# Performance work log

Hardware: AMD Instinct MI355X
Metric: run time of the kernel (lower is better)

## Reference

```python
import jax, jax.numpy as jnp
import numpy as np

EMBED_DIM = 512
NUM_HEADS = 8
HEAD_DIM = EMBED_DIM // NUM_HEADS  # 64
LN_EPS = 1e-5
SEQ = 2048
BATCH = 2


def sparsemax(z):
    """Sparsemax over last axis: euclidean projection of each row onto the simplex."""
    K = z.shape[-1]
    z_sorted = -jnp.sort(-z, axis=-1)                      # descending
    z_cumsum = jnp.cumsum(z_sorted, axis=-1)
    r = jnp.arange(1, K + 1, dtype=z.dtype)
    support = r * z_sorted > (z_cumsum - 1.0)
    k_int = jnp.sum(support.astype(jnp.int32), axis=-1, keepdims=True)  # support size >= 1
    tau_sum = jnp.take_along_axis(z_cumsum, k_int - 1, axis=-1)
    tau = (tau_sum - 1.0) / k_int.astype(z.dtype)
    return jnp.maximum(z - tau, 0.0)


def layer_norm(x, eps=LN_EPS):
    # per-head pattern normalization over head_dim, no affine (normalize_pattern_affine=False)
    mu = jnp.mean(x, axis=-1, keepdims=True)
    var = jnp.mean(jnp.square(x - mu), axis=-1, keepdims=True)
    return (x - mu) * jax.lax.rsqrt(var + eps)


def setup_inputs() -> dict:
    key = jax.random.key(0)
    ks = jax.random.split(key, 6)
    E = EMBED_DIM
    return {
        "query": jax.random.normal(ks[0], (SEQ, BATCH, E), dtype=jnp.float32),
        "key": jax.random.normal(ks[1], (SEQ, BATCH, E), dtype=jnp.float32),
        "value": jax.random.normal(ks[2], (SEQ, BATCH, E), dtype=jnp.float32),
        "in_proj_weight": 0.02 * jax.random.normal(ks[3], (3 * E, E), dtype=jnp.float32),
        "in_proj_bias": jnp.zeros((3 * E,), dtype=jnp.float32),
        "out_proj_weight": 0.02 * jax.random.normal(ks[4], (E, E), dtype=jnp.float32),
        "out_proj_bias": jnp.zeros((E,), dtype=jnp.float32),
        "update_steps_max": 0,  # single association pass
    }


def reference(query, key, value, in_proj_weight, in_proj_bias,
              out_proj_weight, out_proj_bias, update_steps_max):
    L, B, E = query.shape
    S = key.shape[0]
    H, D = NUM_HEADS, HEAD_DIM
    wq, wk, wv = in_proj_weight[:E], in_proj_weight[E:2 * E], in_proj_weight[2 * E:]
    bq, bk, bv = in_proj_bias[:E], in_proj_bias[E:2 * E], in_proj_bias[2 * E:]
    # projections (torch Linear: x @ W.T + b)
    q = (query @ wq.T + bq).reshape(L, B, H, D)
    k = (key @ wk.T + bk).reshape(S, B, H, D)
    v = (value @ wv.T + bv).reshape(S, B, H, D)
    # pattern normalization (normalize_pattern=True, no affine), then attention scaling
    q = layer_norm(q) * (float(D) ** -0.5)
    k = layer_norm(k)
    v = layer_norm(v)
    # association scores [B, H, Lq, Lk]
    scores = jnp.einsum('ibhd,jbhd->bhij', q, k)
    attn = sparsemax(scores)  # sparse='sparsemax' activation over key axis
    out = jnp.einsum('bhij,jbhd->ibhd', attn, v).reshape(L, B, E)
    return out @ out_proj_weight.T + out_proj_bias
```

## Files before the change

### kernel.cpp

```cpp
#include <hip/hip_runtime.h>

#define SEQ   2048
#define BATCH 2
#define EMB   512
#define NH    8
#define HD    64
#define CAP   48

typedef short bf16x8 __attribute__((ext_vector_type(8)));
typedef float f32x4  __attribute__((ext_vector_type(4)));

static __device__ __forceinline__ unsigned short f2bf(float f) {
    unsigned u = __float_as_uint(f);
    unsigned r = (u + 0x7FFF + ((u >> 16) & 1)) >> 16;
    return (unsigned short)r;
}
static __device__ __forceinline__ float bf2f(unsigned short h) {
    return __uint_as_float((unsigned)h << 16);
}

__global__ __launch_bounds__(256) void gemm_qkv_ln(
    const float* __restrict__ query, const float* __restrict__ key_in,
    const float* __restrict__ value,
    const float* __restrict__ ipw, const float* __restrict__ ipb,
    unsigned short* __restrict__ qhi, unsigned short* __restrict__ qlo,
    unsigned short* __restrict__ khi, unsigned short* __restrict__ klo,
    float* __restrict__ vn)
{
    const int z = blockIdx.z;
    const float* X = (z == 0) ? query : (z == 1) ? key_in : value;
    unsigned short* dh = (z == 0) ? qhi : khi;
    unsigned short* dl = (z == 0) ? qlo : klo;
    const float scale = (z == 0) ? 0.125f : 1.0f;

    const int t0  = blockIdx.x * 128;
    const int h   = blockIdx.y;
    const int og0 = z * EMB + h * 64;

    __shared__ float Xs[16][132];
    __shared__ float Ws[16][68];
    __shared__ float Et[128][68];
    __shared__ float mu_s[128], rs_s[128];

    const int tid = threadIdx.x;
    const int tx  = tid & 15;
    const int ty  = tid >> 4;

    float acc[8][4];
#pragma unroll
    for (int i = 0; i < 8; ++i)
#pragma unroll
        for (int j = 0; j < 4; ++j) acc[i][j] = 0.f;

    for (int ck = 0; ck < 32; ++ck) {
        const int c0 = ck * 16;
#pragma unroll
        for (int p = 0; p < 2; ++p) {
            int f  = tid + p * 256;
            int tl = f >> 2, cq = (f & 3) << 2;
            const float4 v = *(const float4*)&X[(size_t)(t0 + tl) * EMB + c0 + cq];
            Xs[cq + 0][tl] = v.x; Xs[cq + 1][tl] = v.y;
            Xs[cq + 2][tl] = v.z; Xs[cq + 3][tl] = v.w;
        }
        {
            int f  = tid;
            int ol = f >> 2, cq = (f & 3) << 2;
            const float4 v = *(const float4*)&ipw[(size_t)(og0 + ol) * EMB + c0 + cq];
            Ws[cq + 0][ol] = v.x; Ws[cq + 1][ol] = v.y;
            Ws[cq + 2][ol] = v.z; Ws[cq + 3][ol] = v.w;
        }
        __syncthreads();
#pragma unroll
        for (int c = 0; c < 16; ++c) {
            const float4 a0 = *(const float4*)&Xs[c][ty * 8];
            const float4 a1 = *(const float4*)&Xs[c][ty * 8 + 4];
            const float4 b  = *(const float4*)&Ws[c][tx * 4];
            const float av[8] = {a0.x, a0.y, a0.z, a0.w, a1.x, a1.y, a1.z, a1.w};
            const float bv[4] = {b.x, b.y, b.z, b.w};
#pragma unroll
            for (int i = 0; i < 8; ++i)
#pragma unroll
                for (int j = 0; j < 4; ++j) acc[i][j] += av[i] * bv[j];
        }
        __syncthreads();
    }

#pragma unroll
    for (int j = 0; j < 4; ++j) {
        const float bj = ipb[og0 + tx * 4 + j];
#pragma unroll
        for (int i = 0; i < 8; ++i) Et[ty * 8 + i][tx * 4 + j] = acc[i][j] + bj;
    }
    __syncthreads();
    if (tid < 128) {
        float s = 0.f;
#pragma unroll
        for (int dq = 0; dq < 64; dq += 4) {
            const float4 v = *(const float4*)&Et[tid][dq];
            s += v.x + v.y + v.z + v.w;
        }
        const float mu = s * (1.0f / 64.0f);
        float vs = 0.f;
#pragma unroll
        for (int dq = 0; dq < 64; dq += 4) {
            const float4 v = *(const float4*)&Et[tid][dq];
            const float a = v.x - mu, b = v.y - mu, c = v.z - mu, d = v.w - mu;
            vs += a * a + b * b + c * c + d * d;
        }
        mu_s[tid] = mu;
        rs_s[tid] = rsqrtf(vs * (1.0f / 64.0f) + 1e-5f);
    }
    __syncthreads();
#pragma unroll
    for (int p = 0; p < 8; ++p) {
        int f  = tid + p * 256;
        int tl = f >> 4, dq = (f & 15) << 2;
        const float4 v = *(const float4*)&Et[tl][dq];
        const float mu = mu_s[tl];
        const float rs = rs_s[tl] * scale;
        float x0 = (v.x - mu) * rs, x1 = (v.y - mu) * rs;
        float x2 = (v.z - mu) * rs, x3 = (v.w - mu) * rs;
        const int tg = t0 + tl;
        const int ii = tg >> 1;
        const int b  = tg & 1;
        const size_t base = ((size_t)(b * NH + h) * SEQ + ii) * 64 + dq;
        if (z == 2) {
            float4 o; o.x = x0; o.y = x1; o.z = x2; o.w = x3;
            *(float4*)&vn[base] = o;
        } else {
            ushort4 hi, lo;
            hi.x = f2bf(x0); lo.x = f2bf(x0 - bf2f(hi.x));
            hi.y = f2bf(x1); lo.y = f2bf(x1 - bf2f(hi.y));
            hi.z = f2bf(x2); lo.z = f2bf(x2 - bf2f(hi.z));
            hi.w = f2bf(x3); lo.w = f2bf(x3 - bf2f(hi.w));
            *(ushort4*)&dh[base] = hi;
            *(ushort4*)&dl[base] = lo;
        }
    }
}

__global__ __launch_bounds__(512, 4) void attn_sparsemax_mfma(
    const unsigned short* __restrict__ qhi, const unsigned short* __restrict__ qlo,
    const unsigned short* __restrict__ khi, const unsigned short* __restrict__ klo,
    const float* __restrict__ vn, float* __restrict__ ao)
{
    __shared__ float          plist[16][8][CAP];
    __shared__ unsigned short jlist[16][8][CAP];
    __shared__ short          lcnt[16][8];
    __shared__ float          wred[8][16];
    __shared__ float          wcnt[8][16];
    __shared__ float          O_lds[16][64];

    const int tid = threadIdx.x;
    const int w   = tid >> 6;
    const int l   = tid & 63;
    const int c   = l & 15;
    const int g   = l >> 4;
    const int bh  = blockIdx.y;
    const int q0  = blockIdx.x * 16;

    const size_t bhoff = (size_t)bh * SEQ * 64;
    const unsigned short* qh = qhi + bhoff;
    const unsigned short* ql = qlo + bhoff;
    const unsigned short* kh = khi + bhoff;
    const unsigned short* kl = klo + bhoff;
    const float*          vb = vn  + bhoff;

    for (int f = tid; f < 16 * 64; f += 512) ((float*)O_lds)[f] = 0.f;

    const size_t qrow = (size_t)(q0 + c) * 64 + g * 8;
    const bf16x8 ah0 = *(const bf16x8*)&qh[qrow];
    const bf16x8 ah1 = *(const bf16x8*)&qh[qrow + 32];
    const bf16x8 al0 = *(const bf16x8*)&ql[qrow];
    const bf16x8 al1 = *(const bf16x8*)&ql[qrow + 32];

    f32x4 acc[16];
#pragma unroll
    for (int nf = 0; nf < 16; ++nf) acc[nf] = (f32x4){0.f, 0.f, 0.f, 0.f};

    const int n0base = w * 256;
#pragma unroll
    for (int nf = 0; nf < 16; ++nf) {
        const size_t krow = (size_t)(n0base + nf * 16 + c) * 64 + g * 8;
        f32x4 t = acc[nf];
        const bf16x8 bh0 = *(const bf16x8*)&kh[krow];
        t = __builtin_amdgcn_mfma_f32_16x16x32_bf16(ah0, bh0, t, 0, 0, 0);
        t = __builtin_amdgcn_mfma_f32_16x16x32_bf16(al0, bh0, t, 0, 0, 0);
        const bf16x8 bh1 = *(const bf16x8*)&kh[krow + 32];
        t = __builtin_amdgcn_mfma_f32_16x16x32_bf16(ah1, bh1, t, 0, 0, 0);
        t = __builtin_amdgcn_mfma_f32_16x16x32_bf16(al1, bh1, t, 0, 0, 0);
        const bf16x8 bl0 = *(const bf16x8*)&kl[krow];
        t = __builtin_amdgcn_mfma_f32_16x16x32_bf16(ah0, bl0, t, 0, 0, 0);
        const bf16x8 bl1 = *(const bf16x8*)&kl[krow + 32];
        t = __builtin_amdgcn_mfma_f32_16x16x32_bf16(ah1, bl1, t, 0, 0, 0);
        acc[nf] = t;
    }

    float mj[4];
#pragma unroll
    for (int j = 0; j < 4; ++j) {
        float m = acc[0][j];
#pragma unroll
        for (int nf = 1; nf < 16; ++nf) m = fmaxf(m, acc[nf][j]);
#pragma unroll
        for (int d = 1; d <= 8; d <<= 1) m = fmaxf(m, __shfl_xor(m, d));
        mj[j] = m;
    }
    if (c == 0) {
#pragma unroll
        for (int j = 0; j < 4; ++j) wred[w][g * 4 + j] = mj[j];
    }
    __syncthreads();

    float tau[4];
    int   cprev[4];
#pragma unroll
    for (int j = 0; j < 4; ++j) {
        float m = wred[0][g * 4 + j];
#pragma unroll
        for (int ww = 1; ww < 8; ++ww) m = fmaxf(m, wred[ww][g * 4 + j]);
        tau[j]   = m - 1.0f;
        cprev[j] = -1;
    }

    for (int it = 0; it < 32; ++it) {
        __syncthreads();
        float sj[4], cj[4];
#pragma unroll
        for (int j = 0; j < 4; ++j) {
            float s = 0.f, cn = 0.f;
#pragma unroll
            for (int nf = 0; nf < 16; ++nf) {
                const float v = acc[nf][j];
                if (v > tau[j]) { s += v; cn += 1.f; }
            }
#pragma unroll
            for (int d = 1; d <= 8; d <<= 1) {
                s  += __shfl_xor(s, d);
                cn += __shfl_xor(cn, d);
            }
            sj[j] = s; cj[j] = cn;
        }
        if (c == 0) {
#pragma unroll
            for (int j = 0; j < 4; ++j) {
                wred[w][g * 4 + j] = sj[j];
                wcnt[w][g * 4 + j] = cj[j];
            }
        }
        __syncthreads();
        int changed = 0;
#pragma unroll
        for (int j = 0; j < 4; ++j) {
            float S = 0.f, C = 0.f;
#pragma unroll
            for (int ww = 0; ww < 8; ++ww) {
                S += wred[ww][g * 4 + j];
                C += wcnt[ww][g * 4 + j];
            }
            tau[j] = (S - 1.0f) / C;
            const int Ci = (int)C;
            changed |= (Ci != cprev[j]);
            cprev[j] = Ci;
        }
        if (!__any(changed)) break;
    }

    int cnt[4] = {0, 0, 0, 0};
#pragma unroll
    for (int nf = 0; nf < 16; ++nf) {
#pragma unroll
        for (int j = 0; j < 4; ++j) {
            const float p  = acc[nf][j] - tau[j];
            const bool  on = p > 0.f;
            const unsigned long long mask = __ballot(on);
            const unsigned sub = (unsigned)((mask >> (g * 16)) & 0xFFFFull);
            const int pre = __popc(sub & ((1u << c) - 1u));
            const int pos = cnt[j] + pre;
            const int r   = g * 4 + j;
            const int col = n0base + nf * 16 + c;
            if (on) {
                if (pos < CAP) {
                    jlist[r][w][pos] = (unsigned short)col;
                    plist[r][w][pos] = p;
                } else {
                    for (int d = 0; d < 64; ++d)
                        atomicAdd(&O_lds[r][d], p * vb[(size_t)col * 64 + d]);
                }
            }
            cnt[j] += __popc(sub);
        }
    }
    if (c == 0) {
#pragma unroll
        for (int j = 0; j < 4; ++j)
            lcnt[g * 4 + j][w] = (short)min(cnt[j], CAP);
    }
    __syncthreads();

    float oacc[2] = {0.f, 0.f};
#pragma unroll
    for (int rr = 0; rr < 2; ++rr) {
        const int r = w * 2 + rr;
#pragma unroll 1
        for (int sw = 0; sw < 8; ++sw) {
            const int n = lcnt[r][sw];
#pragma unroll 1
            for (int e = 0; e < n; ++e) {
                const float p = plist[r][sw][e];
                const int   j = jlist[r][sw][e];
                oacc[rr] += p * vb[(size_t)j * 64 + l];
            }
        }
    }
    const int b = bh >> 3, h = bh & 7;
#pragma unroll
    for (int rr = 0; rr < 2; ++rr) {
        const int r = w * 2 + rr;
        const int i = q0 + r;
        ao[(size_t)(i * BATCH + b) * EMB + h * 64 + l] = oacc[rr] + O_lds[r][l];
    }
}

__global__ __launch_bounds__(256) void gemm_out_proj(
    const float* __restrict__ X, const float* __restrict__ W,
    const float* __restrict__ bias, float* __restrict__ out)
{
    const int t0 = blockIdx.x * 128;
    const int o0 = blockIdx.y * 64;

    __shared__ float Xs[16][132];
    __shared__ float Ws[16][68];

    const int tid = threadIdx.x;
    const int tx  = tid & 15;
    const int ty  = tid >> 4;

    float acc[8][4];
#pragma unroll
    for (int i = 0; i < 8; ++i)
#pragma unroll
        for (int j = 0; j < 4; ++j) acc[i][j] = 0.f;

    for (int ck = 0; ck < 32; ++ck) {
        const int c0 = ck * 16;
#pragma unroll
        for (int p = 0; p < 2; ++p) {
            int f  = tid + p * 256;
            int tl = f >> 2, cq = (f & 3) << 2;
            const float4 v = *(const float4*)&X[(size_t)(t0 + tl) * EMB + c0 + cq];
            Xs[cq + 0][tl] = v.x; Xs[cq + 1][tl] = v.y;
            Xs[cq + 2][tl] = v.z; Xs[cq + 3][tl] = v.w;
        }
        {
            int f  = tid;
            int ol = f >> 2, cq = (f & 3) << 2;
            const float4 v = *(const float4*)&W[(size_t)(o0 + ol) * EMB + c0 + cq];
            Ws[cq + 0][ol] = v.x; Ws[cq + 1][ol] = v.y;
            Ws[cq + 2][ol] = v.z; Ws[cq + 3][ol] = v.w;
        }
        __syncthreads();
#pragma unroll
        for (int cc = 0; cc < 16; ++cc) {
            const float4 a0 = *(const float4*)&Xs[cc][ty * 8];
            const float4 a1 = *(const float4*)&Xs[cc][ty * 8 + 4];
            const float4 b  = *(const float4*)&Ws[cc][tx * 4];
            const float av[8] = {a0.x, a0.y, a0.z, a0.w, a1.x, a1.y, a1.z, a1.w};
            const float bv[4] = {b.x, b.y, b.z, b.w};
#pragma unroll
            for (int i = 0; i < 8; ++i)
#pragma unroll
                for (int j = 0; j < 4; ++j) acc[i][j] += av[i] * bv[j];
        }
        __syncthreads();
    }

    const float b0 = bias[o0 + tx * 4 + 0];
    const float b1 = bias[o0 + tx * 4 + 1];
    const float b2 = bias[o0 + tx * 4 + 2];
    const float b3 = bias[o0 + tx * 4 + 3];
#pragma unroll
    for (int i = 0; i < 8; ++i) {
        float4 o;
        o.x = acc[i][0] + b0; o.y = acc[i][1] + b1;
        o.z = acc[i][2] + b2; o.w = acc[i][3] + b3;
        *(float4*)&out[(size_t)(t0 + ty * 8 + i) * EMB + o0 + tx * 4] = o;
    }
}

extern "C" void kernel_launch(void* const* d_in, const int* in_sizes, int n_in,
                              void* d_out, int out_size, void* d_ws, size_t ws_size,
                              hipStream_t stream)
{
    const float* query = (const float*)d_in[0];
    const float* key_  = (const float*)d_in[1];
    const float* value = (const float*)d_in[2];
    const float* ipw   = (const float*)d_in[3];
    const float* ipb   = (const float*)d_in[4];
    const float* opw   = (const float*)d_in[5];
    const float* opb   = (const float*)d_in[6];

    char* ws = (char*)d_ws;
    const size_t NTOK = (size_t)BATCH * NH * SEQ * 64;
    unsigned short* qhi = (unsigned short*)(ws);
    unsigned short* qlo = (unsigned short*)(ws + 4  * 1024 * 1024);
    unsigned short* khi = (unsigned short*)(ws + 8  * 1024 * 1024);
    unsigned short* klo = (unsigned short*)(ws + 12 * 1024 * 1024);
    float*          vnp = (float*)(ws + 16 * 1024 * 1024);
    float*          aop = (float*)(ws + 24 * 1024 * 1024);
    (void)NTOK; (void)ws_size;
    float* out = (float*)d_out;

    gemm_qkv_ln<<<dim3(32, 8, 3), 256, 0, stream>>>(
        query, key_, value, ipw, ipb, qhi, qlo, khi, klo, vnp);
    attn_sparsemax_mfma<<<dim3(SEQ / 16, BATCH * NH), 512, 0, stream>>>(
        qhi, qlo, khi, klo, vnp, aop);
    gemm_out_proj<<<dim3(32, 8), 256, 0, stream>>>(aop, opw, opb, out);
}
```

Before: 444.5 us.

## Move projections to split-bf16 MFMA and restructure sparsemax support lists

Adds a pre-pass that splits the inputs and both weight matrices into bf16 hi/lo pairs. The QKV projection with LayerNorm and the output projection now run on 3-term bf16 MFMA instead of scalar FP32 FMA loops, and the LayerNorm reductions use wave shuffles. The attention kernel now builds one per-row support list with a prefix-counted offset per wave and a larger capacity, unrolls the value gather, and remaps blocks so heads are spread across XCDs. This adds an extra conversion pass and extra workspace traffic, and the projections drop LDS staging in favour of direct global fragment loads.

```diff
diff --git a/kernel.cpp b/kernel.cpp
--- a/kernel.cpp
+++ b/kernel.cpp
@@ -5,166 +5,201 @@
 #define EMB   512
 #define NH    8
 #define HD    64
-#define CAP   48
+#define CAPR  320
 
 typedef short bf16x8 __attribute__((ext_vector_type(8)));
 typedef float f32x4  __attribute__((ext_vector_type(4)));
-
-static __device__ __forceinline__ unsigned short f2bf(float f) {
+typedef unsigned short ushort_t;
+
+static __device__ __forceinline__ ushort_t f2bf(float f) {
     unsigned u = __float_as_uint(f);
     unsigned r = (u + 0x7FFF + ((u >> 16) & 1)) >> 16;
-    return (unsigned short)r;
-}
-static __device__ __forceinline__ float bf2f(unsigned short h) {
+    return (ushort_t)r;
+}
+static __device__ __forceinline__ float bf2f(ushort_t h) {
     return __uint_as_float((unsigned)h << 16);
 }
 
-__global__ __launch_bounds__(256) void gemm_qkv_ln(
-    const float* __restrict__ query, const float* __restrict__ key_in,
-    const float* __restrict__ value,
-    const float* __restrict__ ipw, const float* __restrict__ ipb,
-    unsigned short* __restrict__ qhi, unsigned short* __restrict__ qlo,
-    unsigned short* __restrict__ khi, unsigned short* __restrict__ klo,
+#define Q4   524288
+#define K4   1048576
+#define V4   1572864
+#define IW4  1769472
+#define TOT4 1835008
+__global__ __launch_bounds__(256) void convert_split(
+    const float* __restrict__ q, const float* __restrict__ k,
+    const float* __restrict__ v, const float* __restrict__ ipw,
+    const float* __restrict__ opw,
+    ushort_t* __restrict__ xqh, ushort_t* __restrict__ xql,
+    ushort_t* __restrict__ xkh, ushort_t* __restrict__ xkl,
+    ushort_t* __restrict__ xvh, ushort_t* __restrict__ xvl,
+    ushort_t* __restrict__ iwh, ushort_t* __restrict__ iwl,
+    ushort_t* __restrict__ owh, ushort_t* __restrict__ owl)
+{
+    for (long f = (long)blockIdx.x * 256 + threadIdx.x; f < TOT4;
+         f += (long)gridDim.x * 256) {
+        const float* src; ushort_t *dh, *dl; long o;
+        if      (f < Q4)  { src = q;   dh = xqh; dl = xql; o = f; }
+        else if (f < K4)  { src = k;   dh = xkh; dl = xkl; o = f - Q4; }
+        else if (f < V4)  { src = v;   dh = xvh; dl = xvl; o = f - K4; }
+        else if (f < IW4) { src = ipw; dh = iwh; dl = iwl; o = f - V4; }
+        else              { src = opw; dh = owh; dl = owl; o = f - IW4; }
+        const float4 x = ((const float4*)src)[o];
+        ushort4 hi, lo;
+        hi.x = f2bf(x.x); lo.x = f2bf(x.x - bf2f(hi.x));
+        hi.y = f2bf(x.y); lo.y = f2bf(x.y - bf2f(hi.y));
+        hi.z = f2bf(x.z); lo.z = f2bf(x.z - bf2f(hi.z));
+        hi.w = f2bf(x.w); lo.w = f2bf(x.w - bf2f(hi.w));
+        ((ushort4*)dh)[o] = hi;
+        ((ushort4*)dl)[o] = lo;
+    }
+}
+
+__global__ __launch_bounds__(256, 4) void gemm_qkv_ln_mfma(
+    const ushort_t* __restrict__ xqh, const ushort_t* __restrict__ xql,
+    const ushort_t* __restrict__ xkh, const ushort_t* __restrict__ xkl,
+    const ushort_t* __restrict__ xvh, const ushort_t* __restrict__ xvl,
+    const ushort_t* __restrict__ iwh, const ushort_t* __restrict__ iwl,
+    const float* __restrict__ ipb,
+    ushort_t* __restrict__ qhi, ushort_t* __restrict__ qlo,
+    ushort_t* __restrict__ khi, ushort_t* __restrict__ klo,
     float* __restrict__ vn)
 {
     const int z = blockIdx.z;
-    const float* X = (z == 0) ? query : (z == 1) ? key_in : value;
-    unsigned short* dh = (z == 0) ? qhi : khi;
-    unsigned short* dl = (z == 0) ? qlo : klo;
+    const ushort_t* Ah = (z == 0) ? xqh : (z == 1) ? xkh : xvh;
+    const ushort_t* Al = (z == 0) ? xql : (z == 1) ? xkl : xvl;
+    ushort_t* dh = (z == 0) ? qhi : khi;
+    ushort_t* dl = (z == 0) ? qlo : klo;
     const float scale = (z == 0) ? 0.125f : 1.0f;
 
     const int t0  = blockIdx.x * 128;
     const int h   = blockIdx.y;
     const int og0 = z * EMB + h * 64;
-
-    __shared__ float Xs[16][132];
-    __shared__ float Ws[16][68];
-    __shared__ float Et[128][68];
-    __shared__ float mu_s[128], rs_s[128];
-
-    const int tid = threadIdx.x;
-    const int tx  = tid & 15;
-    const int ty  = tid >> 4;
-
-    float acc[8][4];
-#pragma unroll
-    for (int i = 0; i < 8; ++i)
-#pragma unroll
-        for (int j = 0; j < 4; ++j) acc[i][j] = 0.f;
-
-    for (int ck = 0; ck < 32; ++ck) {
-        const int c0 = ck * 16;
-#pragma unroll
-        for (int p = 0; p < 2; ++p) {
-            int f  = tid + p * 256;
-            int tl = f >> 2, cq = (f & 3) << 2;
-            const float4 v = *(const float4*)&X[(size_t)(t0 + tl) * EMB + c0 + cq];
-            Xs[cq + 0][tl] = v.x; Xs[cq + 1][tl] = v.y;
-            Xs[cq + 2][tl] = v.z; Xs[cq + 3][tl] = v.w;
-        }
-        {
-            int f  = tid;
-            int ol = f >> 2, cq = (f & 3) << 2;
-            const float4 v = *(const float4*)&ipw[(size_t)(og0 + ol) * EMB + c0 + cq];
-            Ws[cq + 0][ol] = v.x; Ws[cq + 1][ol] = v.y;
-            Ws[cq + 2][ol] = v.z; Ws[cq + 3][ol] = v.w;
-        }
-        __syncthreads();
-#pragma unroll
-        for (int c = 0; c < 16; ++c) {
-            const float4 a0 = *(const float4*)&Xs[c][ty * 8];
-            const float4 a1 = *(const float4*)&Xs[c][ty * 8 + 4];
-            const float4 b  = *(const float4*)&Ws[c][tx * 4];
-            const float av[8] = {a0.x, a0.y, a0.z, a0.w, a1.x, a1.y, a1.z, a1.w};
-            const float bv[4] = {b.x, b.y, b.z, b.w};
-#pragma unroll
-            for (int i = 0; i < 8; ++i)
-#pragma unroll
-                for (int j = 0; j < 4; ++j) acc[i][j] += av[i] * bv[j];
-        }
-        __syncthreads();
-    }
-
-#pragma unroll
-    for (int j = 0; j < 4; ++j) {
-        const float bj = ipb[og0 + tx * 4 + j];
-#pragma unroll
-        for (int i = 0; i < 8; ++i) Et[ty * 8 + i][tx * 4 + j] = acc[i][j] + bj;
-    }
-    __syncthreads();
-    if (tid < 128) {
-        float s = 0.f;
-#pragma unroll
-        for (int dq = 0; dq < 64; dq += 4) {
-            const float4 v = *(const float4*)&Et[tid][dq];
-            s += v.x + v.y + v.z + v.w;
-        }
-        const float mu = s * (1.0f / 64.0f);
-        float vs = 0.f;
-#pragma unroll
-        for (int dq = 0; dq < 64; dq += 4) {
-            const float4 v = *(const float4*)&Et[tid][dq];
-            const float a = v.x - mu, b = v.y - mu, c = v.z - mu, d = v.w - mu;
-            vs += a * a + b * b + c * c + d * d;
-        }
-        mu_s[tid] = mu;
-        rs_s[tid] = rsqrtf(vs * (1.0f / 64.0f) + 1e-5f);
-    }
-    __syncthreads();
-#pragma unroll
-    for (int p = 0; p < 8; ++p) {
-        int f  = tid + p * 256;
-        int tl = f >> 4, dq = (f & 15) << 2;
-        const float4 v = *(const float4*)&Et[tl][dq];
-        const float mu = mu_s[tl];
-        const float rs = rs_s[tl] * scale;
-        float x0 = (v.x - mu) * rs, x1 = (v.y - mu) * rs;
-        float x2 = (v.z - mu) * rs, x3 = (v.w - mu) * rs;
-        const int tg = t0 + tl;
-        const int ii = tg >> 1;
-        const int b  = tg & 1;
-        const size_t base = ((size_t)(b * NH + h) * SEQ + ii) * 64 + dq;
-        if (z == 2) {
-            float4 o; o.x = x0; o.y = x1; o.z = x2; o.w = x3;
-            *(float4*)&vn[base] = o;
-        } else {
-            ushort4 hi, lo;
-            hi.x = f2bf(x0); lo.x = f2bf(x0 - bf2f(hi.x));
-            hi.y = f2bf(x1); lo.y = f2bf(x1 - bf2f(hi.y));
-            hi.z = f2bf(x2); lo.z = f2bf(x2 - bf2f(hi.z));
-            hi.w = f2bf(x3); lo.w = f2bf(x3 - bf2f(hi.w));
-            *(ushort4*)&dh[base] = hi;
-            *(ushort4*)&dl[base] = lo;
-        }
-    }
-}
-
-__global__ __launch_bounds__(512, 4) void attn_sparsemax_mfma(
-    const unsigned short* __restrict__ qhi, const unsigned short* __restrict__ qlo,
-    const unsigned short* __restrict__ khi, const unsigned short* __restrict__ klo,
-    const float* __restrict__ vn, float* __restrict__ ao)
-{
-    __shared__ float          plist[16][8][CAP];
-    __shared__ unsigned short jlist[16][8][CAP];
-    __shared__ short          lcnt[16][8];
-    __shared__ float          wred[8][16];
-    __shared__ float          wcnt[8][16];
-    __shared__ float          O_lds[16][64];
 
     const int tid = threadIdx.x;
     const int w   = tid >> 6;
     const int l   = tid & 63;
     const int c   = l & 15;
     const int g   = l >> 4;
-    const int bh  = blockIdx.y;
-    const int q0  = blockIdx.x * 16;
+
+    f32x4 acc[2][4];
+#pragma unroll
+    for (int mf = 0; mf < 2; ++mf)
+#pragma unroll
+        for (int nf = 0; nf < 4; ++nf) acc[mf][nf] = (f32x4){0.f, 0.f, 0.f, 0.f};
+
+    const int arow0 = t0 + w * 32 + c;
+#pragma unroll
+    for (int ks = 0; ks < 16; ++ks) {
+        const int k0 = ks * 32 + g * 8;
+        bf16x8 ah[2], al[2], bh[4], bl[4];
+#pragma unroll
+        for (int mf = 0; mf < 2; ++mf) {
+            const size_t r = (size_t)(arow0 + mf * 16) * EMB + k0;
+            ah[mf] = *(const bf16x8*)&Ah[r];
+            al[mf] = *(const bf16x8*)&Al[r];
+        }
+#pragma unroll
+        for (int nf = 0; nf < 4; ++nf) {
+            const size_t r = (size_t)(og0 + nf * 16 + c) * EMB + k0;
+            bh[nf] = *(const bf16x8*)&iwh[r];
+            bl[nf] = *(const bf16x8*)&iwl[r];
+        }
+#pragma unroll
+        for (int mf = 0; mf < 2; ++mf)
+#pragma unroll
+            for (int nf = 0; nf < 4; ++nf) {
+                f32x4 t = acc[mf][nf];
+                t = __builtin_amdgcn_mfma_f32_16x16x32_bf16(ah[mf], bh[nf], t, 0, 0, 0);
+                t = __builtin_amdgcn_mfma_f32_16x16x32_bf16(al[mf], bh[nf], t, 0, 0, 0);
+                t = __builtin_amdgcn_mfma_f32_16x16x32_bf16(ah[mf], bl[nf], t, 0, 0, 0);
+                acc[mf][nf] = t;
+            }
+    }
+
+#pragma unroll
+    for (int nf = 0; nf < 4; ++nf) {
+        const float bj = ipb[og0 + nf * 16 + c];
+#pragma unroll
+        for (int mf = 0; mf < 2; ++mf)
+#pragma unroll
+            for (int j = 0; j < 4; ++j) acc[mf][nf][j] += bj;
+    }
+
+#pragma unroll
+    for (int mf = 0; mf < 2; ++mf) {
+        float mu[4], rs[4];
+#pragma unroll
+        for (int j = 0; j < 4; ++j) {
+            float s = acc[mf][0][j] + acc[mf][1][j] + acc[mf][2][j] + acc[mf][3][j];
+#pragma unroll
+            for (int d = 1; d <= 8; d <<= 1) s += __shfl_xor(s, d);
+            mu[j] = s * (1.0f / 64.0f);
+        }
+#pragma unroll
+        for (int j = 0; j < 4; ++j) {
+            float t = 0.f;
+#pragma unroll
+            for (int nf = 0; nf < 4; ++nf) {
+                const float dv = acc[mf][nf][j] - mu[j];
+                t += dv * dv;
+            }
+#pragma unroll
+            for (int d = 1; d <= 8; d <<= 1) t += __shfl_xor(t, d);
+            rs[j] = rsqrtf(t * (1.0f / 64.0f) + 1e-5f) * scale;
+        }
+#pragma unroll
+        for (int j = 0; j < 4; ++j) {
+            const int tg = t0 + w * 32 + mf * 16 + g * 4 + j;
+            const int ii = tg >> 1;
+            const int b  = tg & 1;
+            const size_t base = ((size_t)(b * NH + h) * SEQ + ii) * 64 + c;
+#pragma unroll
+            for (int nf = 0; nf < 4; ++nf) {
+                const float val = (acc[mf][nf][j] - mu[j]) * rs[j];
+                const size_t a = base + nf * 16;
+                if (z == 2) {
+                    vn[a] = val;
+                } else {
+                    const ushort_t hi = f2bf(val);
+                    dh[a] = hi;
+                    dl[a] = f2bf(val - bf2f(hi));
+                }
+            }
+        }
+    }
+}
+
+__global__ __launch_bounds__(512, 4) void attn_sparsemax_mfma(
+    const ushort_t* __restrict__ qhi, const ushort_t* __restrict__ qlo,
+    const ushort_t* __restrict__ khi, const ushort_t* __restrict__ klo,
+    const float* __restrict__ vn,
+    ushort_t* __restrict__ aoh, ushort_t* __restrict__ aol)
+{
+    __shared__ float    plist[16][CAPR];
+    __shared__ ushort_t jlist[16][CAPR];
+    __shared__ int      lcnt[16][8];
+    __shared__ float    wred[8][16];
+    __shared__ float    wcnt[8][16];
+    __shared__ float    O_lds[16][64];
+
+    const int tid = threadIdx.x;
+    const int w   = tid >> 6;
+    const int l   = tid & 63;
+    const int c   = l & 15;
+    const int g   = l >> 4;
+
+    const int wgid = blockIdx.x;
+    const int xcd  = wgid & 7;
+    const int idx  = wgid >> 3;
+    const int bh   = xcd + 8 * (idx & 1);
+    const int q0   = (idx >> 1) * 16;
 
     const size_t bhoff = (size_t)bh * SEQ * 64;
-    const unsigned short* qh = qhi + bhoff;
-    const unsigned short* ql = qlo + bhoff;
-    const unsigned short* kh = khi + bhoff;
-    const unsigned short* kl = klo + bhoff;
-    const float*          vb = vn  + bhoff;
+    const ushort_t* qh = qhi + bhoff;
+    const ushort_t* ql = qlo + bhoff;
+    const ushort_t* kh = khi + bhoff;
+    const ushort_t* kl = klo + bhoff;
+    const float*    vb = vn  + bhoff;
 
     for (int f = tid; f < 16 * 64; f += 512) ((float*)O_lds)[f] = 0.f;
 
@@ -271,121 +306,141 @@
     for (int nf = 0; nf < 16; ++nf) {
 #pragma unroll
         for (int j = 0; j < 4; ++j) {
+            const bool on = (acc[nf][j] - tau[j]) > 0.f;
+            const unsigned long long mask = __ballot(on);
+            cnt[j] += __popc((unsigned)((mask >> (g * 16)) & 0xFFFFull));
+        }
+    }
+    if (c == 0) {
+#pragma unroll
+        for (int j = 0; j < 4; ++j) lcnt[g * 4 + j][w] = cnt[j];
+    }
+    __syncthreads();
+
+    int base[4];
+#pragma unroll
+    for (int j = 0; j < 4; ++j) {
+        const int r = g * 4 + j;
+        int b = 0;
+        for (int ww = 0; ww < w; ++ww) b += lcnt[r][ww];
+        base[j] = b;
+    }
+    int run[4] = {0, 0, 0, 0};
+#pragma unroll
+    for (int nf = 0; nf < 16; ++nf) {
+#pragma unroll
+        for (int j = 0; j < 4; ++j) {
             const float p  = acc[nf][j] - tau[j];
             const bool  on = p > 0.f;
             const unsigned long long mask = __ballot(on);
             const unsigned sub = (unsigned)((mask >> (g * 16)) & 0xFFFFull);
-            const int pre = __popc(sub & ((1u << c) - 1u));
-            const int pos = cnt[j] + pre;
-            const int r   = g * 4 + j;
-            const int col = n0base + nf * 16 + c;
             if (on) {
-                if (pos < CAP) {
-                    jlist[r][w][pos] = (unsigned short)col;
-                    plist[r][w][pos] = p;
+                const int pos = base[j] + run[j] + __popc(sub & ((1u << c) - 1u));
+                const int r   = g * 4 + j;
+                const int col = n0base + nf * 16 + c;
+                if (pos < CAPR) {
+                    jlist[r][pos] = (ushort_t)col;
+                    plist[r][pos] = p;
                 } else {
                     for (int d = 0; d < 64; ++d)
                         atomicAdd(&O_lds[r][d], p * vb[(size_t)col * 64 + d]);
                 }
             }
-            cnt[j] += __popc(sub);
-        }
-    }
-    if (c == 0) {
-#pragma unroll
-        for (int j = 0; j < 4; ++j)
-            lcnt[g * 4 + j][w] = (short)min(cnt[j], CAP);
+            run[j] += __popc(sub);
+        }
     }
     __syncthreads();
 
-    float oacc[2] = {0.f, 0.f};
+    const int bq = bh >> 3, hc = bh & 7;
 #pragma unroll
     for (int rr = 0; rr < 2; ++rr) {
         const int r = w * 2 + rr;
-#pragma unroll 1
-        for (int sw = 0; sw < 8; ++sw) {
-            const int n = lcnt[r][sw];
-#pragma unroll 1
-            for (int e = 0; e < n; ++e) {
-                const float p = plist[r][sw][e];
-                const int   j = jlist[r][sw][e];
-                oacc[rr] += p * vb[(size_t)j * 64 + l];
-            }
-        }
-    }
-    const int b = bh >> 3, h = bh & 7;
-#pragma unroll
-    for (int rr = 0; rr < 2; ++rr) {
-        const int r = w * 2 + rr;
+        int n = 0;
+#pragma unroll
+        for (int ww = 0; ww < 8; ++ww) n += lcnt[r][ww];
+        n = min(n, CAPR);
+        float a0 = 0.f, a1 = 0.f, a2 = 0.f, a3 = 0.f;
+        int e = 0;
+        for (; e + 4 <= n; e += 4) {
+            const int   j0 = jlist[r][e + 0], j1 = jlist[r][e + 1];
+            const int   j2 = jlist[r][e + 2], j3 = jlist[r][e + 3];
+            const float p0 = plist[r][e + 0], p1 = plist[r][e + 1];
+            const float p2 = plist[r][e + 2], p3 = plist[r][e + 3];
+            a0 += p0 * vb[(size_t)j0 * 64 + l];
+            a1 += p1 * vb[(size_t)j1 * 64 + l];
+            a2 += p2 * vb[(size_t)j2 * 64 + l];
+            a3 += p3 * vb[(size_t)j3 * 64 + l];
+        }
+        for (; e < n; ++e)
+            a0 += plist[r][e] * vb[(size_t)jlist[r][e] * 64 + l];
+        const float val = a0 + a1 + a2 + a3 + O_lds[r][l];
         const int i = q0 + r;
-        ao[(size_t)(i * BATCH + b) * EMB + h * 64 + l] = oacc[rr] + O_lds[r][l];
-    }
-}
-
-__global__ __launch_bounds__(256) void gemm_out_proj(
-    const float* __restrict__ X, const float* __restrict__ W,
-    const float* __restrict__ bias, float* __restrict__ out)
+        const size_t oa = (size_t)(i * BATCH + bq) * EMB + hc * 64 + l;
+        const ushort_t hi = f2bf(val);
+        aoh[oa] = hi;
+        aol[oa] = f2bf(val - bf2f(hi));
+    }
+}
+
+__global__ __launch_bounds__(256, 4) void gemm_out_mfma(
+    const ushort_t* __restrict__ aoh, const ushort_t* __restrict__ aol,
+    const ushort_t* __restrict__ owh, const ushort_t* __restrict__ owl,
+    const float* __restrict__ opb, float* __restrict__ out)
 {
     const int t0 = blockIdx.x * 128;
     const int o0 = blockIdx.y * 64;
 
-    __shared__ float Xs[16][132];
-    __shared__ float Ws[16][68];
-
     const int tid = threadIdx.x;
-    const int tx  = tid & 15;
-    const int ty  = tid >> 4;
-
-    float acc[8][4];
-#pragma unroll
-    for (int i = 0; i < 8; ++i)
-#pragma unroll
-        for (int j = 0; j < 4; ++j) acc[i][j] = 0.f;
-
-    for (int ck = 0; ck < 32; ++ck) {
-        const int c0 = ck * 16;
-#pragma unroll
-        for (int p = 0; p < 2; ++p) {
-            int f  = tid + p * 256;
-            int tl = f >> 2, cq = (f & 3) << 2;
-            const float4 v = *(const float4*)&X[(size_t)(t0 + tl) * EMB + c0 + cq];
-            Xs[cq + 0][tl] = v.x; Xs[cq + 1][tl] = v.y;
-            Xs[cq + 2][tl] = v.z; Xs[cq + 3][tl] = v.w;
-        }
-        {
-            int f  = tid;
-            int ol = f >> 2, cq = (f & 3) << 2;
-            const float4 v = *(const float4*)&W[(size_t)(o0 + ol) * EMB + c0 + cq];
-            Ws[cq + 0][ol] = v.x; Ws[cq + 1][ol] = v.y;
-            Ws[cq + 2][ol] = v.z; Ws[cq + 3][ol] = v.w;
-        }
-        __syncthreads();
-#pragma unroll
-        for (int cc = 0; cc < 16; ++cc) {
-            const float4 a0 = *(const float4*)&Xs[cc][ty * 8];
-            const float4 a1 = *(const float4*)&Xs[cc][ty * 8 + 4];
-            const float4 b  = *(const float4*)&Ws[cc][tx * 4];
-            const float av[8] = {a0.x, a0.y, a0.z, a0.w, a1.x, a1.y, a1.z, a1.w};
-            const float bv[4] = {b.x, b.y, b.z, b.w};
-#pragma unroll
-            for (int i = 0; i < 8; ++i)
-#pragma unroll
-                for (int j = 0; j < 4; ++j) acc[i][j] += av[i] * bv[j];
-        }
-        __syncthreads();
-    }
-
-    const float b0 = bias[o0 + tx * 4 + 0];
-    const float b1 = bias[o0 + tx * 4 + 1];
-    const float b2 = bias[o0 + tx * 4 + 2];
-    const float b3 = bias[o0 + tx * 4 + 3];
-#pragma unroll
-    for (int i = 0; i < 8; ++i) {
-        float4 o;
-        o.x = acc[i][0] + b0; o.y = acc[i][1] + b1;
-        o.z = acc[i][2] + b2; o.w = acc[i][3] + b3;
-        *(float4*)&out[(size_t)(t0 + ty * 8 + i) * EMB + o0 + tx * 4] = o;
-    }
+    const int w   = tid >> 6;
+    const int l   = tid & 63;
+    const int c   = l & 15;
+    const int g   = l >> 4;
+
+    f32x4 acc[2][4];
+#pragma unroll
+    for (int mf = 0; mf < 2; ++mf)
+#pragma unroll
+        for (int nf = 0; nf < 4; ++nf) acc[mf][nf] = (f32x4){0.f, 0.f, 0.f, 0.f};
+
+    const int arow0 = t0 + w * 32 + c;
+#pragma unroll
+    for (int ks = 0; ks < 16; ++ks) {
+        const int k0 = ks * 32 + g * 8;
+        bf16x8 ah[2], al[2], bh[4], bl[4];
+#pragma unroll
+        for (int mf = 0; mf < 2; ++mf) {
+            const size_t r = (size_t)(arow0 + mf * 16) * EMB + k0;
+            ah[mf] = *(const bf16x8*)&aoh[r];
+            al[mf] = *(const bf16x8*)&aol[r];
+        }
+#pragma unroll
+        for (int nf = 0; nf < 4; ++nf) {
+            const size_t r = (size_t)(o0 + nf * 16 + c) * EMB + k0;
+            bh[nf] = *(const bf16x8*)&owh[r];
+            bl[nf] = *(const bf16x8*)&owl[r];
+        }
+#pragma unroll
+        for (int mf = 0; mf < 2; ++mf)
+#pragma unroll
+            for (int nf = 0; nf < 4; ++nf) {
+                f32x4 t = acc[mf][nf];
+                t = __builtin_amdgcn_mfma_f32_16x16x32_bf16(ah[mf], bh[nf], t, 0, 0, 0);
+                t = __builtin_amdgcn_mfma_f32_16x16x32_bf16(al[mf], bh[nf], t, 0, 0, 0);
+                t = __builtin_amdgcn_mfma_f32_16x16x32_bf16(ah[mf], bl[nf], t, 0, 0, 0);
+                acc[mf][nf] = t;
+            }
+    }
+
+#pragma unroll
+    for (int mf = 0; mf < 2; ++mf)
+#pragma unroll
+        for (int j = 0; j < 4; ++j) {
+            const int tg = t0 + w * 32 + mf * 16 + g * 4 + j;
+#pragma unroll
+            for (int nf = 0; nf < 4; ++nf)
+                out[(size_t)tg * EMB + o0 + nf * 16 + c] =
+                    acc[mf][nf][j] + opb[o0 + nf * 16 + c];
+        }
 }
 
 extern "C" void kernel_launch(void* const* d_in, const int* in_sizes, int n_in,
@@ -401,19 +456,34 @@
     const float* opb   = (const float*)d_in[6];
 
     char* ws = (char*)d_ws;
-    const size_t NTOK = (size_t)BATCH * NH * SEQ * 64;
-    unsigned short* qhi = (unsigned short*)(ws);
-    unsigned short* qlo = (unsigned short*)(ws + 4  * 1024 * 1024);
-    unsigned short* khi = (unsigned short*)(ws + 8  * 1024 * 1024);
-    unsigned short* klo = (unsigned short*)(ws + 12 * 1024 * 1024);
-    float*          vnp = (float*)(ws + 16 * 1024 * 1024);
-    float*          aop = (float*)(ws + 24 * 1024 * 1024);
-    (void)NTOK; (void)ws_size;
+    const size_t MB = 1024 * 1024;
+    ushort_t* xqh = (ushort_t*)(ws + 0 * MB);
+    ushort_t* xql = (ushort_t*)(ws + 4 * MB);
+    ushort_t* xkh = (ushort_t*)(ws + 8 * MB);
+    ushort_t* xkl = (ushort_t*)(ws + 12 * MB);
+    ushort_t* xvh = (ushort_t*)(ws + 16 * MB);
+    ushort_t* xvl = (ushort_t*)(ws + 20 * MB);
+    ushort_t* qhi = (ushort_t*)(ws + 24 * MB);
+    ushort_t* qlo = (ushort_t*)(ws + 28 * MB);
+    ushort_t* khi = (ushort_t*)(ws + 32 * MB);
+    ushort_t* klo = (ushort_t*)(ws + 36 * MB);
+    float*    vn  = (float*)   (ws + 40 * MB);
+    ushort_t* iwh = (ushort_t*)(ws + 48 * MB);
+    ushort_t* iwl = (ushort_t*)(ws + 50 * MB);
+    ushort_t* owh = (ushort_t*)(ws + 52 * MB);
+    ushort_t* owl = (ushort_t*)(ws + 53 * MB);
+    ushort_t* aoh = (ushort_t*)(ws + 0 * MB);
+    ushort_t* aol = (ushort_t*)(ws + 4 * MB);
     float* out = (float*)d_out;
-
-    gemm_qkv_ln<<<dim3(32, 8, 3), 256, 0, stream>>>(
-        query, key_, value, ipw, ipb, qhi, qlo, khi, klo, vnp);
-    attn_sparsemax_mfma<<<dim3(SEQ / 16, BATCH * NH), 512, 0, stream>>>(
-        qhi, qlo, khi, klo, vnp, aop);
-    gemm_out_proj<<<dim3(32, 8), 256, 0, stream>>>(aop, opw, opb, out);
-}
+    (void)ws_size;
+
+    convert_split<<<2048, 256, 0, stream>>>(
+        query, key_, value, ipw, opw,
+        xqh, xql, xkh, xkl, xvh, xvl, iwh, iwl, owh, owl);
+    gemm_qkv_ln_mfma<<<dim3(32, 8, 3), 256, 0, stream>>>(
+        xqh, xql, xkh, xkl, xvh, xvl, iwh, iwl, ipb, qhi, qlo, khi, klo, vn);
+    attn_sparsemax_mfma<<<2048, 512, 0, stream>>>(
+        qhi, qlo, khi, klo, vn, aoh, aol);
+    gemm_out_mfma<<<dim3(32, 8), 256, 0, stream>>>(
+        aoh, aol, owh, owl, opb, out);
+}
```

Measured after the change: 499.9 us. 12.5% more time.
